# Kernel tuning notes

Measured on AMD Instinct MI355X. Metric: run time of the kernel, lower is better.

Reference implementation:

```python
import jax, jax.numpy as jnp
import numpy as np

D_MODEL = 1024
NUM_HEADS = 16
HEAD_DIM = D_MODEL // NUM_HEADS
B, S = 2, 2048


def setup_inputs() -> dict:
    key = jax.random.key(0)
    ks = jax.random.split(key, 8)
    scale = 1.0 / np.sqrt(D_MODEL)
    inp = {
        "query": jax.random.normal(ks[0], (B, S, D_MODEL), jnp.float32),
        "key": jax.random.normal(ks[1], (B, S, D_MODEL), jnp.float32),
        "value": jax.random.normal(ks[2], (B, S, D_MODEL), jnp.float32),
        # causal mask, broadcastable over batch and heads
        "mask": jnp.tril(jnp.ones((S, S), dtype=bool))[None, None, :, :],
        # torch nn.Linear weights: y = x @ W.T (+ b)
        "Wq": jax.random.normal(ks[3], (D_MODEL, D_MODEL), jnp.float32) * scale,
        "Wk": jax.random.normal(ks[4], (D_MODEL, D_MODEL), jnp.float32) * scale,
        "Wv": jax.random.normal(ks[5], (D_MODEL, D_MODEL), jnp.float32) * scale,
        "Wo": jax.random.normal(ks[6], (D_MODEL, D_MODEL), jnp.float32) * scale,
        "bo": jax.random.normal(ks[7], (D_MODEL,), jnp.float32) * scale,
    }
    return inp


def _split_heads(x):
    b, s, _ = x.shape
    return x.reshape(b, s, NUM_HEADS, HEAD_DIM).transpose(0, 2, 1, 3)  # [B,H,S,Dh]


def reference(query, key, value, mask, Wq, Wk, Wv, Wo, bo):
    q = _split_heads(query @ Wq.T)
    k = _split_heads(key @ Wk.T)
    v = _split_heads(value @ Wv.T)
    scores = jnp.einsum("bhqd,bhkd->bhqk", q, k) / jnp.sqrt(jnp.float32(HEAD_DIM))
    scores = jnp.where(mask, scores, jnp.float32(-jnp.inf))
    attn = jax.nn.softmax(scores, axis=-1)
    out = jnp.einsum("bhqk,bhkd->bhqd", attn, v)  # [B,H,S,Dh]
    out = out.transpose(0, 2, 1, 3).reshape(query.shape[0], q.shape[2], D_MODEL)
    return out @ Wo.T + bo
```

## Files before the change

kernel.cpp:

```cpp
#include <hip/hip_runtime.h>
#include <hip/hip_bf16.h>

#define DM   1024
#define NH   16
#define HD   64
#define SEQ  2048
#define BATCH 2
#define MTOT (BATCH*SEQ)

typedef unsigned short u16;
typedef __attribute__((ext_vector_type(8))) short bf16x8;
typedef __attribute__((ext_vector_type(4))) float f32x4;

#define SC2F 0.1803368801111464f

__device__ __forceinline__ float bf2f(u16 h) {
  union { unsigned int i; float f; } u; u.i = ((unsigned int)h) << 16; return u.f;
}
__device__ __forceinline__ u16 f2bf(float f) {
  union { float f; unsigned int i; } u; u.f = f;
  unsigned int r = u.i + 0x7fffu + ((u.i >> 16) & 1u);
  return (u16)(r >> 16);
}
__device__ __forceinline__ unsigned int pk2(float lo, float hi) {
  union { float f; unsigned int u; } a, b; a.f = lo; b.f = hi;
  return ((a.u + 0x8000u) >> 16) | ((b.u + 0x8000u) & 0xFFFF0000u);
}

__device__ __forceinline__ uint4 load8_bf16(const void* base, size_t elemOff, bool isf32) {
  if (!isf32) return *(const uint4*)((const u16*)base + elemOff);
  const float* f = (const float*)base + elemOff;
  f32x4 a = *(const f32x4*)f;
  f32x4 b = *(const f32x4*)(f + 4);
  union { u16 h[8]; uint4 v; } r;
  r.h[0]=f2bf(a[0]); r.h[1]=f2bf(a[1]); r.h[2]=f2bf(a[2]); r.h[3]=f2bf(a[3]);
  r.h[4]=f2bf(b[0]); r.h[5]=f2bf(b[1]); r.h[6]=f2bf(b[2]); r.h[7]=f2bf(b[3]);
  return r.v;
}

__global__ __launch_bounds__(256) void prep(
    const void* __restrict__ q, const void* __restrict__ k, const void* __restrict__ v,
    const void* __restrict__ wq, const void* __restrict__ wk, const void* __restrict__ wv,
    const void* __restrict__ wo, const void* __restrict__ bo,
    u16* __restrict__ Xq, u16* __restrict__ Xk, u16* __restrict__ Xv,
    u16* __restrict__ Wqb, u16* __restrict__ Wkb, u16* __restrict__ Wvb, u16* __restrict__ Wob,
    float* __restrict__ biasf, int* __restrict__ flag_out)
{
  const int tid = threadIdx.x;
  __shared__ int cnts[4];
  {
    const u16* qs = (const u16*)q;
    int e0 = (qs[tid*2]   >> 7) & 0xFF;
    int e1 = (qs[tid*2+1] >> 7) & 0xFF;
    int c = ((e0 >= 0x6E && e0 <= 0x8F) ? 1 : 0) + ((e1 >= 0x6E && e1 <= 0x8F) ? 1 : 0);
    c += __shfl_xor(c, 1);  c += __shfl_xor(c, 2);  c += __shfl_xor(c, 4);
    c += __shfl_xor(c, 8);  c += __shfl_xor(c, 16); c += __shfl_xor(c, 32);
    if ((tid & 63) == 0) cnts[tid >> 6] = c;
  }
  __syncthreads();
  const bool isf32 = (cnts[0] + cnts[1] + cnts[2] + cnts[3]) < 400;

  const int z = blockIdx.z;
  if (z == 7) {
    if (blockIdx.x == 0) {
      if (tid == 0) *flag_out = isf32 ? 0 : 1;
      for (int i = tid; i < DM; i += 256)
        biasf[i] = isf32 ? ((const float*)bo)[i] : bf2f(((const u16*)bo)[i]);
    }
    return;
  }
  const void* src; u16* dst; size_t n;
  switch (z) {
    case 0: src=q;  dst=Xq;  n=(size_t)MTOT*DM; break;
    case 1: src=k;  dst=Xk;  n=(size_t)MTOT*DM; break;
    case 2: src=v;  dst=Xv;  n=(size_t)MTOT*DM; break;
    case 3: src=wq; dst=Wqb; n=(size_t)DM*DM;   break;
    case 4: src=wk; dst=Wkb; n=(size_t)DM*DM;   break;
    case 5: src=wv; dst=Wvb; n=(size_t)DM*DM;   break;
    default: src=wo; dst=Wob; n=(size_t)DM*DM;  break;
  }
  const size_t stride = (size_t)gridDim.x * 256 * 8;
  for (size_t i = ((size_t)blockIdx.x * 256 + tid) * 8; i < n; i += stride)
    *(uint4*)(dst + i) = load8_bf16(src, i, isf32);
}

__device__ __forceinline__ void gld16(const u16* g, u16* l) {
  __builtin_amdgcn_global_load_lds(
      (const __attribute__((address_space(1))) void*)g,
      (__attribute__((address_space(3))) void*)l, 16, 0, 0);
}

__global__ __launch_bounds__(256) void gemm_qkv(
    const u16* __restrict__ X0, const u16* __restrict__ X1, const u16* __restrict__ X2,
    const u16* __restrict__ W0, const u16* __restrict__ W1, const u16* __restrict__ W2,
    u16* __restrict__ F0, u16* __restrict__ F1, u16* __restrict__ F2)
{
  __shared__ u16 As[128*32];
  __shared__ u16 Bs[128*32];

  const int zz = blockIdx.z;
  const u16* X = (zz==0) ? X0 : ((zz==1) ? X1 : X2);
  const u16* W = (zz==0) ? W0 : ((zz==1) ? W1 : W2);
  u16* outF    = (zz==0) ? F0 : ((zz==1) ? F1 : F2);

  const int tid = threadIdx.x;
  const int wave = tid >> 6, lane = tid & 63, quad = lane >> 4, l16 = lane & 15;
  const int wr = wave >> 1, wc = wave & 1;
  const int m0 = blockIdx.x * 128, n0 = blockIdx.y * 128;

  const int sg = ((lane & 3) ^ ((lane >> 3) & 3)) * 8;
  const int rS = wave*32 + (lane >> 2);
  const u16* gA0 = X + (size_t)(m0 + rS)*DM + sg;
  const u16* gA1 = X + (size_t)(m0 + rS + 16)*DM + sg;
  const u16* gB0 = W + (size_t)(n0 + rS)*DM + sg;
  const u16* gB1 = W + (size_t)(n0 + rS + 16)*DM + sg;
  u16* lA0 = &As[wave*1024];
  u16* lA1 = &As[wave*1024 + 512];
  u16* lB0 = &Bs[wave*1024];
  u16* lB1 = &Bs[wave*1024 + 512];

  const int xslot8 = (quad ^ ((l16 >> 1) & 3)) * 8;

  f32x4 acc[4][4];
#pragma unroll
  for (int i = 0; i < 4; i++)
#pragma unroll
    for (int j = 0; j < 4; j++) { acc[i][j][0]=0.f; acc[i][j][1]=0.f; acc[i][j][2]=0.f; acc[i][j][3]=0.f; }

  for (int k0 = 0; k0 < DM; k0 += 32) {
    __syncthreads();
    gld16(gA0 + k0, lA0);
    gld16(gA1 + k0, lA1);
    gld16(gB0 + k0, lB0);
    gld16(gB1 + k0, lB1);
    __syncthreads();

    bf16x8 af[4], bfr[4];
#pragma unroll
    for (int fr = 0; fr < 4; fr++)
      af[fr] = *(const bf16x8*)&As[(wr*64 + fr*16 + l16)*32 + xslot8];
#pragma unroll
    for (int fc = 0; fc < 4; fc++)
      bfr[fc] = *(const bf16x8*)&Bs[(wc*64 + fc*16 + l16)*32 + xslot8];
#pragma unroll
    for (int fr = 0; fr < 4; fr++)
#pragma unroll
      for (int fc = 0; fc < 4; fc++)
        acc[fr][fc] = __builtin_amdgcn_mfma_f32_16x16x32_bf16(af[fr], bfr[fc], acc[fr][fc], 0, 0, 0);
  }

  if (zz == 2) {
    __shared__ u16 Ts[64*128];
    const int bb = m0 >> 11;
    const int s0 = m0 & (SEQ-1);
#pragma unroll
    for (int p = 0; p < 2; p++) {
      __syncthreads();
      if (wc == p) {
#pragma unroll
        for (int fr = 0; fr < 4; fr++) {
#pragma unroll
          for (int fc = 0; fc < 4; fc++) {
            const int dl = fc*16 + l16;
            const int sb = wr*64 + fr*16 + quad*4;
            const int slot = (sb >> 3) ^ (dl & 15);
            u16* rowp = &Ts[dl*128 + slot*8 + (sb & 7)];
            *(unsigned int*)(rowp)     = pk2(acc[fr][fc][0], acc[fr][fc][1]);
            *(unsigned int*)(rowp + 2) = pk2(acc[fr][fc][2], acc[fr][fc][3]);
          }
        }
      }
      __syncthreads();
      const int dl2 = tid >> 2, ch4 = tid & 3;
      const int hh = (n0 + p*64) >> 6;
      u16* dst = outF + ((size_t)(bb*NH + hh)*HD + dl2)*SEQ + s0 + ch4*32;
#pragma unroll
      for (int j = 0; j < 4; j++) {
        const int slot = (ch4*4 + j) ^ (dl2 & 15);
        *(uint4*)&dst[j*8] = *(const uint4*)&Ts[dl2*128 + slot*8];
      }
    }
    return;
  }

#pragma unroll
  for (int fr = 0; fr < 4; fr++) {
#pragma unroll
    for (int rr = 0; rr < 4; rr++) {
      const int m = m0 + wr*64 + fr*16 + quad*4 + rr;
#pragma unroll
      for (int fc = 0; fc < 4; fc++) {
        const int n = n0 + wc*64 + fc*16 + l16;
        float vv = acc[fr][fc][rr];
        if (zz == 0) vv *= SC2F;
        const int b = m >> 11, s = m & (SEQ-1), h = n >> 6, d = n & (HD-1);
        outF[((size_t)(b*NH + h)*SEQ + s)*HD + d] = f2bf(vv);
      }
    }
  }
}

__global__ __launch_bounds__(256) void gemm_out(
    const u16* __restrict__ X, const u16* __restrict__ W,
    const float* __restrict__ biasf, void* __restrict__ outP,
    const int* __restrict__ dflag)
{
  __shared__ u16 As[128*32];
  __shared__ u16 Bs[64*32];

  const int tid = threadIdx.x;
  const int wave = tid >> 6, lane = tid & 63, quad = lane >> 4, l16 = lane & 15;
  const int wr = wave >> 1, wc = wave & 1;
  const int m0 = blockIdx.x * 128, n0 = blockIdx.y * 64;

  const int sg = ((lane & 3) ^ ((lane >> 3) & 3)) * 8;
  const int rA = wave*32 + (lane >> 2);
  const int rB = wave*16 + (lane >> 2);
  const u16* gA0 = X + (size_t)(m0 + rA)*DM + sg;
  const u16* gA1 = X + (size_t)(m0 + rA + 16)*DM + sg;
  const u16* gB0 = W + (size_t)(n0 + rB)*DM + sg;
  u16* lA0 = &As[wave*1024];
  u16* lA1 = &As[wave*1024 + 512];
  u16* lB0 = &Bs[wave*512];

  const int xslot8 = (quad ^ ((l16 >> 1) & 3)) * 8;

  f32x4 acc[4][2];
#pragma unroll
  for (int i = 0; i < 4; i++)
#pragma unroll
    for (int j = 0; j < 2; j++) { acc[i][j][0]=0.f; acc[i][j][1]=0.f; acc[i][j][2]=0.f; acc[i][j][3]=0.f; }

  for (int k0 = 0; k0 < DM; k0 += 32) {
    __syncthreads();
    gld16(gA0 + k0, lA0);
    gld16(gA1 + k0, lA1);
    gld16(gB0 + k0, lB0);
    __syncthreads();

    bf16x8 af[4], bfr[2];
#pragma unroll
    for (int fr = 0; fr < 4; fr++)
      af[fr] = *(const bf16x8*)&As[(wr*64 + fr*16 + l16)*32 + xslot8];
#pragma unroll
    for (int fc = 0; fc < 2; fc++)
      bfr[fc] = *(const bf16x8*)&Bs[(wc*32 + fc*16 + l16)*32 + xslot8];
#pragma unroll
    for (int fr = 0; fr < 4; fr++)
#pragma unroll
      for (int fc = 0; fc < 2; fc++)
        acc[fr][fc] = __builtin_amdgcn_mfma_f32_16x16x32_bf16(af[fr], bfr[fc], acc[fr][fc], 0, 0, 0);
  }

  const bool isf32 = (*dflag == 0);
#pragma unroll
  for (int fr = 0; fr < 4; fr++) {
#pragma unroll
    for (int rr = 0; rr < 4; rr++) {
      const int m = m0 + wr*64 + fr*16 + quad*4 + rr;
#pragma unroll
      for (int fc = 0; fc < 2; fc++) {
        const int n = n0 + wc*32 + fc*16 + l16;
        float vv = acc[fr][fc][rr] + biasf[n];
        if (isf32) ((float*)outP)[(size_t)m*DM + n] = vv;
        else       ((u16*)outP)[(size_t)m*DM + n]   = f2bf(vv);
      }
    }
  }
}

__global__ __launch_bounds__(256) void attn_mfma(
    const u16* __restrict__ Qb, const u16* __restrict__ Kb,
    const u16* __restrict__ Vtb,
    u16* __restrict__ Opart, float* __restrict__ mlpart)
{
  __shared__ u16 Qs[64*64];
  __shared__ u16 Ks[64*64];
  __shared__ u16 Vs[64*64];
  __shared__ u16 Ps[4][16][72];

  const int bh = blockIdx.x;
  const int pr = blockIdx.y, z = blockIdx.z;
  const u16* Qp = Qb  + (size_t)bh * SEQ * HD;
  const u16* Kp = Kb  + (size_t)bh * SEQ * HD;
  const u16* Vp = Vtb + (size_t)bh * HD * SEQ;

  const int tid  = threadIdx.x;
  const int wave = tid >> 6, lane = tid & 63, quad = lane >> 4, l16 = lane & 15;

  const int i0 = wave*128 + lane, i1 = i0 + 64;
  const int r0 = i0 >> 3, c0 = (i0 & 7) ^ (r0 & 7);
  const int r1 = i1 >> 3, c1 = (i1 & 7) ^ (r1 & 7);
  const int kq_off0 = r0*HD + c0*8;
  const int kq_off1 = r1*HD + c1*8;
  const int v_off0  = r0*SEQ + c0*8;
  const int v_off1  = r1*SEQ + c1*8;
  u16* ldsQ0 = &Qs[wave*1024]; u16* ldsQ1 = &Qs[wave*1024 + 512];
  u16* ldsK0 = &Ks[wave*1024]; u16* ldsK1 = &Ks[wave*1024 + 512];
  u16* ldsV0 = &Vs[wave*1024]; u16* ldsV1 = &Vs[wave*1024 + 512];

  const int l7 = l16 & 7;

  for (int ph = 0; ph < 2; ph++) {
    const int qt = ph ? (31 - pr) : pr;
    const int n = qt + 1, half = (n + 1) >> 1;
    const int klo = z ? half : 0, khi = z ? n : half;
    const int q0 = qt * 64;

    __syncthreads();
    gld16(Qp + q0*HD + kq_off0, ldsQ0);
    gld16(Qp + q0*HD + kq_off1, ldsQ1);

    const int ql = wave*16 + l16;
    const int qg = q0 + ql;
    f32x4 O[4];
#pragma unroll
    for (int u = 0; u < 4; u++) { O[u][0]=0.f; O[u][1]=0.f; O[u][2]=0.f; O[u][3]=0.f; }
    float mi = -__builtin_inff(), li = 0.f;

    for (int kt = klo; kt < khi; kt++) {
      __syncthreads();
      gld16(Kp + kt*(64*HD) + kq_off0, ldsK0);
      gld16(Kp + kt*(64*HD) + kq_off1, ldsK1);
      gld16(Vp + kt*64 + v_off0, ldsV0);
      gld16(Vp + kt*64 + v_off1, ldsV1);
      __syncthreads();

      f32x4 st[4];
#pragma unroll
      for (int t = 0; t < 4; t++) { st[t][0]=0.f; st[t][1]=0.f; st[t][2]=0.f; st[t][3]=0.f; }
#pragma unroll
      for (int s = 0; s < 2; s++) {
        const int ch = s*4 + quad;
        bf16x8 bq = *(const bf16x8*)&Qs[(ql*8 + (ch ^ l7))*8];
#pragma unroll
        for (int t = 0; t < 4; t++) {
          bf16x8 ak = *(const bf16x8*)&Ks[((t*16 + l16)*8 + (ch ^ l7))*8];
          st[t] = __builtin_amdgcn_mfma_f32_16x16x32_bf16(ak, bq, st[t], 0, 0, 0);
        }
      }

      float v[4][4];
#pragma unroll
      for (int t = 0; t < 4; t++)
#pragma unroll
        for (int r = 0; r < 4; r++) v[t][r] = st[t][r];
      if (kt == qt) {
#pragma unroll
        for (int t = 0; t < 4; t++)
#pragma unroll
          for (int r = 0; r < 4; r++)
            if (kt*64 + t*16 + quad*4 + r > qg) v[t][r] = -__builtin_inff();
      }
      float mx = v[0][0];
#pragma unroll
      for (int t = 0; t < 4; t++)
#pragma unroll
        for (int r = 0; r < 4; r++) mx = fmaxf(mx, v[t][r]);
      mx = fmaxf(mx, __shfl_xor(mx, 16));
      mx = fmaxf(mx, __shfl_xor(mx, 32));
      const float nm = fmaxf(mi, mx);
      const float al = exp2f(mi - nm);
      float ps = 0.f;
#pragma unroll
      for (int t = 0; t < 4; t++) {
        float p0 = exp2f(v[t][0] - nm), p1 = exp2f(v[t][1] - nm);
        float p2 = exp2f(v[t][2] - nm), p3 = exp2f(v[t][3] - nm);
        ps += (p0 + p1) + (p2 + p3);
        uint2 u2; u2.x = pk2(p0, p1); u2.y = pk2(p2, p3);
        *(uint2*)&Ps[wave][l16][t*16 + quad*4] = u2;
      }
      ps += __shfl_xor(ps, 16);
      ps += __shfl_xor(ps, 32);
      li = li * al + ps;
      mi = nm;
#pragma unroll
      for (int u = 0; u < 4; u++) {
        O[u][0] *= al; O[u][1] *= al; O[u][2] *= al; O[u][3] *= al;
      }
      __asm__ volatile("s_waitcnt lgkmcnt(0)" ::: "memory");

#pragma unroll
      for (int s = 0; s < 2; s++) {
        const int ch = s*4 + quad;
        bf16x8 bp = *(const bf16x8*)&Ps[wave][l16][s*32 + quad*8];
#pragma unroll
        for (int u = 0; u < 4; u++) {
          bf16x8 av = *(const bf16x8*)&Vs[((u*16 + l16)*8 + (ch ^ l7))*8];
          O[u] = __builtin_amdgcn_mfma_f32_16x16x32_bf16(av, bp, O[u], 0, 0, 0);
        }
      }
    }

    const int pi = (bh*32 + qt)*2 + z;
    u16* op = Opart + (size_t)pi*4096 + ql*64;
#pragma unroll
    for (int u = 0; u < 4; u++) {
      uint2 u2; u2.x = pk2(O[u][0], O[u][1]); u2.y = pk2(O[u][2], O[u][3]);
      *(uint2*)&op[u*16 + quad*4] = u2;
    }
    if (quad == 0) {
      float2 ml2; ml2.x = mi; ml2.y = li;
      *(float2*)&mlpart[(size_t)pi*128 + ql*2] = ml2;
    }
  }
}

__global__ __launch_bounds__(64) void attn_merge(
    const u16* __restrict__ Opart, const float* __restrict__ mlpart,
    u16* __restrict__ aO)
{
  const int g = blockIdx.x;
  const int bh = g & 31, qt = g >> 5;
  const int b = bh >> 4, h = bh & 15;
  const int t = threadIdx.x;
  const int pi0 = (bh*32 + qt)*2, pi1 = pi0 + 1;

  const float2 ml0 = *(const float2*)&mlpart[(size_t)pi0*128 + t*2];
  const float2 ml1 = *(const float2*)&mlpart[(size_t)pi1*128 + t*2];
  const float M = fmaxf(ml0.x, ml1.x);
  float w0 = exp2f(ml0.x - M), w1 = exp2f(ml1.x - M);
  const float inv = 1.0f / (w0*ml0.y + w1*ml1.y);
  w0 *= inv; w1 *= inv;

  const u16* o0 = Opart + (size_t)pi0*4096 + t*64;
  const u16* o1 = Opart + (size_t)pi1*4096 + t*64;
  u16* out = aO + (size_t)(b*SEQ + qt*64 + t)*DM + h*HD;
#pragma unroll
  for (int d0 = 0; d0 < 64; d0 += 8) {
    union { uint4 v; u16 h[8]; } a, c; union { uint4 v; u16 h[8]; } bb;
    a.v  = *(const uint4*)&o0[d0];
    bb.v = *(const uint4*)&o1[d0];
#pragma unroll
    for (int j = 0; j < 8; j += 2) {
      float x0 = w0*bf2f(a.h[j])   + w1*bf2f(bb.h[j]);
      float x1 = w0*bf2f(a.h[j+1]) + w1*bf2f(bb.h[j+1]);
      unsigned int pk = pk2(x0, x1);
      c.h[j] = (u16)(pk & 0xFFFF); c.h[j+1] = (u16)(pk >> 16);
    }
    *(uint4*)&out[d0] = c.v;
  }
}

extern "C" void kernel_launch(void* const* d_in, const int* in_sizes, int n_in,
                              void* d_out, int out_size, void* d_ws, size_t ws_size,
                              hipStream_t stream) {
  const void* q  = d_in[0];
  const void* k  = d_in[1];
  const void* v  = d_in[2];
  const void* wq = d_in[4];
  const void* wk = d_in[5];
  const void* wv = d_in[6];
  const void* wo = d_in[7];
  const void* bo = d_in[8];

  const size_t TX = (size_t)MTOT*DM;
  const size_t TW = (size_t)DM*DM;
  u16* ws  = (u16*)d_ws;
  u16* Xq  = ws;
  u16* Xk  = ws + TX;
  u16* Xv  = ws + 2*TX;
  u16* Wqb = ws + 3*TX;
  u16* Wkb = Wqb + TW;
  u16* Wvb = Wqb + 2*TW;
  u16* Wob = Wqb + 3*TW;
  u16* Qw  = ws + 3*TX + 4*TW;
  u16* Kw  = Qw + TX;
  u16* Vt  = Qw + 2*TX;
  u16*   Opart  = Xk;
  float* mlpart = (float*)Wqb;
  u16*   aO     = Xq;
  float* biasf  = (float*)(Qw + 3*TX);
  int*   fl     = (int*)(biasf + DM);

  dim3 blk(256);
  prep<<<dim3(512, 1, 8), blk, 0, stream>>>(q, k, v, wq, wk, wv, wo, bo,
      Xq, Xk, Xv, Wqb, Wkb, Wvb, Wob, biasf, fl);
  gemm_qkv<<<dim3(MTOT/128, DM/128, 3), blk, 0, stream>>>(
      Xq, Xk, Xv, Wqb, Wkb, Wvb, Qw, Kw, Vt);
  attn_mfma<<<dim3(BATCH*NH, 16, 2), blk, 0, stream>>>(Qw, Kw, Vt, Opart, mlpart);
  attn_merge<<<dim3(32*32), dim3(64), 0, stream>>>(Opart, mlpart, aO);
  gemm_out<<<dim3(MTOT/128, DM/64), blk, 0, stream>>>(aO, Wob, biasf, d_out, fl);
}
```

Measured before the change: 243.4 us.

## Double-buffer K/V tiles in attention and load Q fragments into registers

The attention kernel now keeps two LDS buffers for K and V and prefetches the next key tile with async global-to-LDS loads while the current tile is computed. It uses explicit vmcnt waits and raw s_barrier in place of the two __syncthreads per iteration. Q fragments are read straight from global memory into registers, which drops the Q LDS buffer. The probability pack switches to the hardware v_cvt_pk_bf16_f32 instruction. The cost is more LDS use and hand-managed wait counts that depend on the load ordering being correct.

```diff
diff --git a/kernel.cpp b/kernel.cpp
--- a/kernel.cpp
+++ b/kernel.cpp
@@ -25,6 +25,11 @@
 __device__ __forceinline__ unsigned int pk2(float lo, float hi) {
   union { float f; unsigned int u; } a, b; a.f = lo; b.f = hi;
   return ((a.u + 0x8000u) >> 16) | ((b.u + 0x8000u) & 0xFFFF0000u);
+}
+__device__ __forceinline__ unsigned int cvtpk(float lo, float hi) {
+  unsigned int r;
+  asm("v_cvt_pk_bf16_f32 %0, %1, %2" : "=v"(r) : "v"(lo), "v"(hi));
+  return r;
 }
 
 __device__ __forceinline__ uint4 load8_bf16(const void* base, size_t elemOff, bool isf32) {
@@ -274,9 +279,8 @@
     const u16* __restrict__ Vtb,
     u16* __restrict__ Opart, float* __restrict__ mlpart)
 {
-  __shared__ u16 Qs[64*64];
-  __shared__ u16 Ks[64*64];
-  __shared__ u16 Vs[64*64];
+  __shared__ u16 Ks[2][64*64];
+  __shared__ u16 Vs[2][64*64];
   __shared__ u16 Ps[4][16][72];
 
   const int bh = blockIdx.x;
@@ -295,68 +299,80 @@
   const int kq_off1 = r1*HD + c1*8;
   const int v_off0  = r0*SEQ + c0*8;
   const int v_off1  = r1*SEQ + c1*8;
-  u16* ldsQ0 = &Qs[wave*1024]; u16* ldsQ1 = &Qs[wave*1024 + 512];
-  u16* ldsK0 = &Ks[wave*1024]; u16* ldsK1 = &Ks[wave*1024 + 512];
-  u16* ldsV0 = &Vs[wave*1024]; u16* ldsV1 = &Vs[wave*1024 + 512];
 
   const int l7 = l16 & 7;
+  const int ql = wave*16 + l16;
+  const int so = wave*1024;
 
   for (int ph = 0; ph < 2; ph++) {
     const int qt = ph ? (31 - pr) : pr;
     const int n = qt + 1, half = (n + 1) >> 1;
     const int klo = z ? half : 0, khi = z ? n : half;
     const int q0 = qt * 64;
-
-    __syncthreads();
-    gld16(Qp + q0*HD + kq_off0, ldsQ0);
-    gld16(Qp + q0*HD + kq_off1, ldsQ1);
-
-    const int ql = wave*16 + l16;
     const int qg = q0 + ql;
+
+    const u16* qrow = Qp + (size_t)qg * HD;
+    const bf16x8 bq0 = *(const bf16x8*)(qrow + quad*8);
+    const bf16x8 bq1 = *(const bf16x8*)(qrow + 32 + quad*8);
+
     f32x4 O[4];
 #pragma unroll
     for (int u = 0; u < 4; u++) { O[u][0]=0.f; O[u][1]=0.f; O[u][2]=0.f; O[u][3]=0.f; }
     float mi = -__builtin_inff(), li = 0.f;
 
+    if (klo < khi) {
+      gld16(Kp + klo*(64*HD) + kq_off0, &Ks[0][so]);
+      gld16(Kp + klo*(64*HD) + kq_off1, &Ks[0][so + 512]);
+      gld16(Vp + klo*64 + v_off0, &Vs[0][so]);
+      gld16(Vp + klo*64 + v_off1, &Vs[0][so + 512]);
+    }
+    asm volatile("" ::: "memory");
+
     for (int kt = klo; kt < khi; kt++) {
-      __syncthreads();
-      gld16(Kp + kt*(64*HD) + kq_off0, ldsK0);
-      gld16(Kp + kt*(64*HD) + kq_off1, ldsK1);
-      gld16(Vp + kt*64 + v_off0, ldsV0);
-      gld16(Vp + kt*64 + v_off1, ldsV1);
-      __syncthreads();
+      const int cb = (kt - klo) & 1;
+      const u16* kb = &Ks[cb][0];
+      const u16* vb = &Vs[cb][0];
+      if (kt + 1 < khi) {
+        u16* kn = &Ks[cb ^ 1][so];
+        u16* vn = &Vs[cb ^ 1][so];
+        gld16(Kp + (kt+1)*(64*HD) + kq_off0, kn);
+        gld16(Kp + (kt+1)*(64*HD) + kq_off1, kn + 512);
+        gld16(Vp + (kt+1)*64 + v_off0, vn);
+        gld16(Vp + (kt+1)*64 + v_off1, vn + 512);
+        asm volatile("s_waitcnt vmcnt(4)" ::: "memory");
+      } else {
+        asm volatile("s_waitcnt vmcnt(0)" ::: "memory");
+      }
+      __builtin_amdgcn_s_barrier();
+      asm volatile("" ::: "memory");
 
       f32x4 st[4];
 #pragma unroll
       for (int t = 0; t < 4; t++) { st[t][0]=0.f; st[t][1]=0.f; st[t][2]=0.f; st[t][3]=0.f; }
 #pragma unroll
       for (int s = 0; s < 2; s++) {
+        const bf16x8 bq = s ? bq1 : bq0;
         const int ch = s*4 + quad;
-        bf16x8 bq = *(const bf16x8*)&Qs[(ql*8 + (ch ^ l7))*8];
 #pragma unroll
         for (int t = 0; t < 4; t++) {
-          bf16x8 ak = *(const bf16x8*)&Ks[((t*16 + l16)*8 + (ch ^ l7))*8];
+          bf16x8 ak = *(const bf16x8*)&kb[((t*16 + l16)*8 + (ch ^ l7))*8];
           st[t] = __builtin_amdgcn_mfma_f32_16x16x32_bf16(ak, bq, st[t], 0, 0, 0);
         }
       }
 
-      float v[4][4];
-#pragma unroll
-      for (int t = 0; t < 4; t++)
-#pragma unroll
-        for (int r = 0; r < 4; r++) v[t][r] = st[t][r];
       if (kt == qt) {
 #pragma unroll
         for (int t = 0; t < 4; t++)
 #pragma unroll
           for (int r = 0; r < 4; r++)
-            if (kt*64 + t*16 + quad*4 + r > qg) v[t][r] = -__builtin_inff();
-      }
-      float mx = v[0][0];
-#pragma unroll
-      for (int t = 0; t < 4; t++)
-#pragma unroll
-        for (int r = 0; r < 4; r++) mx = fmaxf(mx, v[t][r]);
+            if (kt*64 + t*16 + quad*4 + r > qg) st[t][r] = -__builtin_inff();
+      }
+
+      float a0 = fmaxf(fmaxf(st[0][0], st[0][1]), fmaxf(st[0][2], st[0][3]));
+      float a1 = fmaxf(fmaxf(st[1][0], st[1][1]), fmaxf(st[1][2], st[1][3]));
+      float a2 = fmaxf(fmaxf(st[2][0], st[2][1]), fmaxf(st[2][2], st[2][3]));
+      float a3 = fmaxf(fmaxf(st[3][0], st[3][1]), fmaxf(st[3][2], st[3][3]));
+      float mx = fmaxf(fmaxf(a0, a1), fmaxf(a2, a3));
       mx = fmaxf(mx, __shfl_xor(mx, 16));
       mx = fmaxf(mx, __shfl_xor(mx, 32));
       const float nm = fmaxf(mi, mx);
@@ -364,10 +380,10 @@
       float ps = 0.f;
 #pragma unroll
       for (int t = 0; t < 4; t++) {
-        float p0 = exp2f(v[t][0] - nm), p1 = exp2f(v[t][1] - nm);
-        float p2 = exp2f(v[t][2] - nm), p3 = exp2f(v[t][3] - nm);
+        float p0 = exp2f(st[t][0] - nm), p1 = exp2f(st[t][1] - nm);
+        float p2 = exp2f(st[t][2] - nm), p3 = exp2f(st[t][3] - nm);
         ps += (p0 + p1) + (p2 + p3);
-        uint2 u2; u2.x = pk2(p0, p1); u2.y = pk2(p2, p3);
+        uint2 u2; u2.x = cvtpk(p0, p1); u2.y = cvtpk(p2, p3);
         *(uint2*)&Ps[wave][l16][t*16 + quad*4] = u2;
       }
       ps += __shfl_xor(ps, 16);
@@ -378,7 +394,7 @@
       for (int u = 0; u < 4; u++) {
         O[u][0] *= al; O[u][1] *= al; O[u][2] *= al; O[u][3] *= al;
       }
-      __asm__ volatile("s_waitcnt lgkmcnt(0)" ::: "memory");
+      asm volatile("s_waitcnt lgkmcnt(0)" ::: "memory");
 
 #pragma unroll
       for (int s = 0; s < 2; s++) {
@@ -386,10 +402,14 @@
         bf16x8 bp = *(const bf16x8*)&Ps[wave][l16][s*32 + quad*8];
 #pragma unroll
         for (int u = 0; u < 4; u++) {
-          bf16x8 av = *(const bf16x8*)&Vs[((u*16 + l16)*8 + (ch ^ l7))*8];
+          bf16x8 av = *(const bf16x8*)&vb[((u*16 + l16)*8 + (ch ^ l7))*8];
           O[u] = __builtin_amdgcn_mfma_f32_16x16x32_bf16(av, bp, O[u], 0, 0, 0);
         }
       }
+
+      asm volatile("" ::: "memory");
+      __builtin_amdgcn_s_barrier();
+      asm volatile("" ::: "memory");
     }
 
     const int pi = (bh*32 + qt)*2 + z;
```

Result: no change. 245.8 us (+1.0%).
